# Kernel optimization log

Hardware: AMD Instinct MI355X
Metric: run time of the kernel (lower is better)

Reference implementation:

```python
import jax, jax.numpy as jnp
import numpy as np

N = 16384   # num_nodes (also in_channels: identity-style features)
C = 256     # hidden channels
K = 16      # num_classes
E = 524288  # num edges


def gcn_conv(x, src, dst, ew, W, b, num_nodes):
    """PyG GCNConv: linear transform, then sym-normalized scatter-add aggregation.
    Self-loops (weight 1) are appended; norm = d^-1/2[src] * w * d^-1/2[dst]."""
    h = x @ W                                            # [N, out]
    loop = jnp.arange(num_nodes, dtype=src.dtype)
    s = jnp.concatenate([src, loop])
    d = jnp.concatenate([dst, loop])
    w = jnp.concatenate([ew, jnp.ones((num_nodes,), ew.dtype)])
    deg = jax.ops.segment_sum(w, d, num_segments=num_nodes)
    dinv = jnp.where(deg > 0, jax.lax.rsqrt(jnp.maximum(deg, 1e-12)), 0.0)
    norm = dinv[s] * w * dinv[d]                         # [E+N]
    msg = norm[:, None] * h[s]                           # gather + scale
    out = jax.ops.segment_sum(msg, d, num_segments=num_nodes)  # scatter-add
    return out + b


def setup_inputs() -> dict:
    key = jax.random.key(0)
    k1, k2, k3, k4, k5, k6, k7 = jax.random.split(key, 7)
    x = jax.random.normal(k1, (N, N), dtype=jnp.float32)
    edge_index = jax.random.randint(k2, (2, E), 0, N, dtype=jnp.int64)
    edge_weight = jax.random.uniform(k3, (E,), dtype=jnp.float32)
    # GCNConv parameters (glorot-ish scale)
    W1 = jax.random.normal(k4, (N, C), dtype=jnp.float32) / np.sqrt(N)
    b1 = jnp.zeros((C,), jnp.float32)
    W2 = jax.random.normal(k5, (C, K), dtype=jnp.float32) / np.sqrt(C)
    b2 = jnp.zeros((K,), jnp.float32)
    return {"x": x, "edge_index": edge_index, "edge_weight": edge_weight,
            "W1": W1, "b1": b1, "W2": W2, "b2": b2}


def reference(x, edge_index, edge_weight, W1, b1, W2, b2):
    src, dst = edge_index[0], edge_index[1]
    h = gcn_conv(x, src, dst, edge_weight, W1, b1, N)
    h = jax.nn.relu(h)
    # dropout p=0.5 is identity in eval mode (self.training == False)
    out = gcn_conv(h, src, dst, edge_weight, W2, b2, N)
    return out
```

## Files before the change

kernel.cpp:

```cpp
#include <hip/hip_runtime.h>
#include <stdint.h>


namespace {
constexpr int NN = 16384;
constexpr int CH = 256;
constexpr int KC = 16;
constexpr int NE = 524288;
constexpr int KD = 16384;
constexpr int KSPLIT = 4;
constexpr int BM = 128;
constexpr int NT = KD / KSPLIT / 32;
constexpr int ABYTES = BM * 128;
constexpr int BBYTES = 256 * 64;

constexpr size_t OFF_W1T  = 0;
constexpr size_t OFF_HP   = 8388608;
constexpr size_t OFF_HB   = 75497472;
constexpr size_t OFF_OUT1 = 83886080;
constexpr size_t OFF_H2   = 100663296;
constexpr size_t OFF_DEG  = 101711872;
constexpr size_t OFF_CNT  = 101777408;
constexpr size_t OFF_DINV = 101842944;
constexpr size_t OFF_ROWP = 101908480;
constexpr size_t OFF_CUR  = 102039552;
constexpr size_t OFF_COLS = 102105088;
constexpr size_t OFF_NRM  = 104202240;
}

typedef __attribute__((ext_vector_type(8))) short bf16x8;
typedef __attribute__((ext_vector_type(4))) float f32x4;

__device__ __forceinline__ unsigned short f2bf(float f) {
  unsigned int u = __builtin_bit_cast(unsigned int, f);
  u += 0x7fffu + ((u >> 16) & 1u);
  return (unsigned short)(u >> 16);
}
__device__ __forceinline__ float bf2f(unsigned short v) {
  unsigned int u = ((unsigned int)v) << 16;
  return __builtin_bit_cast(float, u);
}

__global__ __launch_bounds__(256)
void k_w1t(const float* __restrict__ w1, unsigned short* __restrict__ w1t) {
  __shared__ float tile[64][65];
  const int t = threadIdx.x;
  const int kb = blockIdx.x * 64;
  const int nb = blockIdx.y * 64;
  const int r = t >> 6;
  const int c = t & 63;
#pragma unroll
  for (int i = 0; i < 16; ++i)
    tile[i * 4 + r][c] = w1[(size_t)(kb + i * 4 + r) * CH + nb + c];
  __syncthreads();
#pragma unroll
  for (int i = 0; i < 16; ++i)
    w1t[(size_t)(nb + i * 4 + r) * KD + kb + c] = f2bf(tile[c][i * 4 + r]);
}

__global__ __launch_bounds__(256)
void k_deg(const int* __restrict__ dst, const float* __restrict__ ew,
           float* __restrict__ deg, int* __restrict__ cnt) {
  const int e = blockIdx.x * 256 + threadIdx.x;
  const int d = dst[e];
  atomicAdd(&deg[d], ew[e]);
  atomicAdd(&cnt[d], 1);
}

__global__ __launch_bounds__(256)
void k_scan(const int* __restrict__ cnt, const float* __restrict__ deg,
            int* __restrict__ rowp, int* __restrict__ curs,
            float* __restrict__ dinv) {
  __shared__ int ps[256];
  const int t = threadIdx.x;
  const int base = t * 64;
  int s = 0;
  for (int j = 0; j < 64; ++j) s += cnt[base + j];
  ps[t] = s;
  for (int j = 0; j < 64; ++j)
    dinv[base + j] = rsqrtf(deg[base + j] + 1.0f);
  __syncthreads();
  int v = s;
  for (int off = 1; off < 256; off <<= 1) {
    int u = (t >= off) ? ps[t - off] : 0;
    __syncthreads();
    v += u;
    ps[t] = v;
    __syncthreads();
  }
  int run = v - s;
  for (int j = 0; j < 64; ++j) {
    int c = cnt[base + j];
    rowp[base + j] = run;
    curs[base + j] = run;
    run += c;
  }
  if (t == 255) rowp[NN] = run;
}

__global__ __launch_bounds__(256)
void k_fill(const int* __restrict__ src, const int* __restrict__ dst,
            const float* __restrict__ ew, const float* __restrict__ dinv,
            int* __restrict__ curs, int* __restrict__ cols, float* __restrict__ nrm) {
  const int e = blockIdx.x * 256 + threadIdx.x;
  const int s = src[e], d = dst[e];
  const int pos = atomicAdd(&curs[d], 1);
  cols[pos] = s;
  nrm[pos] = dinv[s] * ew[e] * dinv[d];
}

__global__ __launch_bounds__(512, 2)
void k_gemm1(const float* __restrict__ x, const unsigned short* __restrict__ w1t,
             float* __restrict__ hp) {
  __shared__ __align__(16) uint8_t lds[4][ABYTES + BBYTES];

  const int tid  = threadIdx.x;
  const int lane = tid & 63;
  const int wave = tid >> 6;
  const int wm   = wave >> 2;
  const int wn   = wave & 3;

  const int bid  = blockIdx.x;
  const int xcd  = bid & 7;
  const int slot = bid >> 3;
  const int kb   = xcd >> 1;
  const int bm0  = (slot * 2 + (xcd & 1)) * BM;
  const int koff = kb * (KD / KSPLIT);

  const float* asrc0 = x + (size_t)(bm0 + 8 * wave + (lane >> 3)) * KD + koff
                         + (((lane & 7) ^ (lane >> 3)) << 2);
  const float* asrc1 = asrc0 + (size_t)64 * KD;
  const unsigned short* bsrc0 = w1t + (size_t)(16 * wave + (lane >> 2)) * KD + koff
                                    + (((lane & 3) ^ ((lane >> 3) & 3)) << 3);
  const unsigned short* bsrc1 = bsrc0 + (size_t)128 * KD;

  const int fr = lane & 15, fg = lane >> 4;
  const int aoff = (((2 * fg) ^ (fr & 7)) << 4);
  const int boff = ((fg ^ ((fr >> 1) & 3)) << 4);
  const int arow = (wm * 64 + fr) * 128 + aoff;
  const int brow = ABYTES + (wn * 64 + fr) * 64 + boff;

  f32x4 acc[4][4] = {};

  auto ISSUE = [&](int tile, int buf) {
    uint8_t* base = &lds[buf][0];
    const float* ap0 = asrc0 + (size_t)tile * 32;
    const float* ap1 = asrc1 + (size_t)tile * 32;
    const unsigned short* bp0 = bsrc0 + (size_t)tile * 32;
    const unsigned short* bp1 = bsrc1 + (size_t)tile * 32;
    __builtin_amdgcn_global_load_lds(
        (const __attribute__((address_space(1))) void*)ap0,
        (__attribute__((address_space(3))) void*)(base + wave * 1024), 16, 0, 0);
    __builtin_amdgcn_global_load_lds(
        (const __attribute__((address_space(1))) void*)ap1,
        (__attribute__((address_space(3))) void*)(base + (wave + 8) * 1024), 16, 0, 0);
    __builtin_amdgcn_global_load_lds(
        (const __attribute__((address_space(1))) void*)bp0,
        (__attribute__((address_space(3))) void*)(base + ABYTES + wave * 1024), 16, 0, 0);
    __builtin_amdgcn_global_load_lds(
        (const __attribute__((address_space(1))) void*)bp1,
        (__attribute__((address_space(3))) void*)(base + ABYTES + 8192 + wave * 1024), 16, 0, 0);
  };

  ISSUE(0, 0);
  ISSUE(1, 1);
  ISSUE(2, 2);

  for (int t = 0; t < NT; ++t) {
    int t3 = t + 3; if (t3 >= NT) t3 -= NT;
    ISSUE(t3, (t + 3) & 3);
    asm volatile("s_waitcnt vmcnt(12)" ::: "memory");
    asm volatile("s_barrier" ::: "memory");
    const uint8_t* Ab = &lds[t & 3][0];
    bf16x8 bfr[4];
#pragma unroll
    for (int ni = 0; ni < 4; ++ni)
      bfr[ni] = *reinterpret_cast<const bf16x8*>(Ab + brow + ni * 1024);
    __builtin_amdgcn_s_setprio(1);
#pragma unroll
    for (int mi = 0; mi < 4; ++mi) {
      const f32x4 lo = *reinterpret_cast<const f32x4*>(Ab + arow + mi * 2048);
      const f32x4 hi = *reinterpret_cast<const f32x4*>(Ab + ((arow + mi * 2048) ^ 16));
      bf16x8 af;
      af[0] = (short)f2bf(lo[0]); af[1] = (short)f2bf(lo[1]);
      af[2] = (short)f2bf(lo[2]); af[3] = (short)f2bf(lo[3]);
      af[4] = (short)f2bf(hi[0]); af[5] = (short)f2bf(hi[1]);
      af[6] = (short)f2bf(hi[2]); af[7] = (short)f2bf(hi[3]);
#pragma unroll
      for (int ni = 0; ni < 4; ++ni)
        acc[mi][ni] = __builtin_amdgcn_mfma_f32_16x16x32_bf16(af, bfr[ni], acc[mi][ni], 0, 0, 0);
    }
    __builtin_amdgcn_s_setprio(0);
    asm volatile("s_barrier" ::: "memory");
  }

  float* hpo = hp + (size_t)kb * NN * CH;
#pragma unroll
  for (int mi = 0; mi < 4; ++mi)
#pragma unroll
    for (int ni = 0; ni < 4; ++ni)
#pragma unroll
      for (int r = 0; r < 4; ++r) {
        const int m = bm0 + wm * 64 + mi * 16 + fg * 4 + r;
        const int n = wn * 64 + ni * 16 + fr;
        hpo[(size_t)m * CH + n] = acc[mi][ni][r];
      }
}

__global__ __launch_bounds__(256)
void k_hred(const float* __restrict__ hp, unsigned short* __restrict__ hb) {
  const size_t i = ((size_t)blockIdx.x * 256 + threadIdx.x) * 8;
  float s[8];
#pragma unroll
  for (int j = 0; j < 8; ++j) s[j] = 0.f;
#pragma unroll
  for (int p = 0; p < KSPLIT; ++p) {
    const float* q = hp + (size_t)p * NN * CH + i;
    const float4 v0 = *reinterpret_cast<const float4*>(q);
    const float4 v1 = *reinterpret_cast<const float4*>(q + 4);
    s[0] += v0.x; s[1] += v0.y; s[2] += v0.z; s[3] += v0.w;
    s[4] += v1.x; s[5] += v1.y; s[6] += v1.z; s[7] += v1.w;
  }
  bf16x8 o;
#pragma unroll
  for (int j = 0; j < 8; ++j) o[j] = (short)f2bf(s[j]);
  *reinterpret_cast<bf16x8*>(hb + i) = o;
}

__global__ __launch_bounds__(256)
void k_agg1(const unsigned short* __restrict__ hb, const int* __restrict__ rowp,
            const int* __restrict__ cols, const float* __restrict__ nrm,
            const float* __restrict__ dinv, const float* __restrict__ b1,
            float* __restrict__ out1) {
  __shared__ float red[4][256];
  const int i = blockIdx.x;
  const int t = threadIdx.x;
  const int w = t >> 6, l = t & 63;
  const int beg = rowp[i], end = rowp[i + 1];
  float a0 = 0.f, a1 = 0.f, a2 = 0.f, a3 = 0.f;
  int e = beg + w;
  for (; e + 4 < end; e += 8) {
    const int s0 = cols[e], s1 = cols[e + 4];
    const float n0 = nrm[e], n1 = nrm[e + 4];
    const ushort4 h0 = *reinterpret_cast<const ushort4*>(hb + (size_t)s0 * CH + l * 4);
    const ushort4 h1 = *reinterpret_cast<const ushort4*>(hb + (size_t)s1 * CH + l * 4);
    a0 += n0 * bf2f(h0.x) + n1 * bf2f(h1.x);
    a1 += n0 * bf2f(h0.y) + n1 * bf2f(h1.y);
    a2 += n0 * bf2f(h0.z) + n1 * bf2f(h1.z);
    a3 += n0 * bf2f(h0.w) + n1 * bf2f(h1.w);
  }
  if (e < end) {
    const int s0 = cols[e];
    const float n0 = nrm[e];
    const ushort4 h0 = *reinterpret_cast<const ushort4*>(hb + (size_t)s0 * CH + l * 4);
    a0 += n0 * bf2f(h0.x); a1 += n0 * bf2f(h0.y);
    a2 += n0 * bf2f(h0.z); a3 += n0 * bf2f(h0.w);
  }
  *reinterpret_cast<float4*>(&red[w][l * 4]) = make_float4(a0, a1, a2, a3);
  __syncthreads();
  const float di = dinv[i];
  float sum = red[0][t] + red[1][t] + red[2][t] + red[3][t]
            + di * di * bf2f(hb[(size_t)i * CH + t]) + b1[t];
  out1[(size_t)i * CH + t] = fmaxf(sum, 0.0f);
}

__global__ __launch_bounds__(256)
void k_gemm2(const float* __restrict__ out1, const float* __restrict__ w2,
             float* __restrict__ h2) {
  __shared__ float xs[16][256];
  __shared__ float ws[256 * 16];
  const int t = threadIdx.x;
  const int n0 = blockIdx.x * 16;
#pragma unroll
  for (int i = 0; i < 16; ++i) ws[i * 256 + t] = w2[i * 256 + t];
#pragma unroll
  for (int i = 0; i < 16; ++i) xs[i][t] = out1[(size_t)(n0 + i) * CH + t];
  __syncthreads();
  const int node = t >> 4, k = t & 15;
  float acc = 0.f;
#pragma unroll 8
  for (int c = 0; c < 256; ++c) acc += xs[node][c] * ws[c * 16 + k];
  h2[(size_t)(n0 + node) * KC + k] = acc;
}

__global__ __launch_bounds__(256)
void k_agg2(const float* __restrict__ h2, const int* __restrict__ rowp,
            const int* __restrict__ cols, const float* __restrict__ nrm,
            const float* __restrict__ dinv, const float* __restrict__ b2,
            float* __restrict__ out) {
  const int i = blockIdx.x * 4 + (threadIdx.x >> 6);
  const int lane = threadIdx.x & 63;
  const int k = lane & 15, g = lane >> 4;
  const int beg = rowp[i], end = rowp[i + 1];
  float acc = 0.f;
  for (int e = beg + g; e < end; e += 4)
    acc += nrm[e] * h2[(size_t)cols[e] * KC + k];
  acc += __shfl_xor(acc, 16);
  acc += __shfl_xor(acc, 32);
  if (g == 0) {
    const float di = dinv[i];
    out[(size_t)i * KC + k] = acc + di * di * h2[(size_t)i * KC + k] + b2[k];
  }
}

extern "C" void kernel_launch(void* const* d_in, const int* in_sizes, int n_in,
                              void* d_out, int out_size, void* d_ws, size_t ws_size,
                              hipStream_t stream) {
  const float* x  = (const float*)d_in[0];
  const int*   ei = (const int*)d_in[1];
  const float* ew = (const float*)d_in[2];
  const float* w1 = (const float*)d_in[3];
  const float* b1 = (const float*)d_in[4];
  const float* w2 = (const float*)d_in[5];
  const float* b2 = (const float*)d_in[6];
  const int* src = ei;
  const int* dst = ei + NE;

  uint8_t* ws = (uint8_t*)d_ws;
  unsigned short* w1t = (unsigned short*)(ws + OFF_W1T);
  float* hp   = (float*)(ws + OFF_HP);
  unsigned short* hb = (unsigned short*)(ws + OFF_HB);
  float* out1 = (float*)(ws + OFF_OUT1);
  float* h2   = (float*)(ws + OFF_H2);
  float* deg  = (float*)(ws + OFF_DEG);
  int*   cnt  = (int*)(ws + OFF_CNT);
  float* dinv = (float*)(ws + OFF_DINV);
  int*   rowp = (int*)(ws + OFF_ROWP);
  int*   curs = (int*)(ws + OFF_CUR);
  int*   cols = (int*)(ws + OFF_COLS);
  float* nrm  = (float*)(ws + OFF_NRM);
  float* out  = (float*)d_out;

  hipMemsetAsync(ws + OFF_DEG, 0, 131072, stream);

  k_w1t <<<dim3(256, 4), 256, 0, stream>>>(w1, w1t);
  k_deg <<<NE / 256, 256, 0, stream>>>(dst, ew, deg, cnt);
  k_scan<<<1, 256, 0, stream>>>(cnt, deg, rowp, curs, dinv);
  k_fill<<<NE / 256, 256, 0, stream>>>(src, dst, ew, dinv, curs, cols, nrm);
  k_gemm1<<<(NN / BM) * KSPLIT, 512, 0, stream>>>(x, w1t, hp);
  k_hred<<<NN * CH / (256 * 8), 256, 0, stream>>>(hp, hb);
  k_agg1<<<NN, 256, 0, stream>>>(hb, rowp, cols, nrm, dinv, b1, out1);
  k_gemm2<<<NN / 16, 256, 0, stream>>>(out1, w2, h2);
  k_agg2<<<NN / 4, 256, 0, stream>>>(h2, rowp, cols, nrm, dinv, b2, out);
}
```

Before: 499.9 us.

## Replace LDS-staged gemm1 with direct register double-buffered fragment loads

The big x@W1 GEMM no longer stages A and B tiles through LDS with global_load_lds and barriers. Each wave now loads its MFMA fragments straight from global memory into registers, double-buffered in software, using nontemporal loads for x and nontemporal stores for the partial outputs. The block tile shrinks to 64 rows with 4 waves, launched as 1024 blocks. This removes LDS traffic and barrier sync, but each wave re-reads W1 fragments from global/L2 with no sharing across waves, and the A loads become strided rows, which may hurt coalescing on a kernel bound by streaming the 1 GB x matrix.

```diff
diff --git a/kernel.cpp b/kernel.cpp
--- a/kernel.cpp
+++ b/kernel.cpp
@@ -9,10 +9,7 @@
 constexpr int NE = 524288;
 constexpr int KD = 16384;
 constexpr int KSPLIT = 4;
-constexpr int BM = 128;
-constexpr int NT = KD / KSPLIT / 32;
-constexpr int ABYTES = BM * 128;
-constexpr int BBYTES = 256 * 64;
+constexpr int NJ = KD / KSPLIT / 32;
 
 constexpr size_t OFF_W1T  = 0;
 constexpr size_t OFF_HP   = 8388608;
@@ -109,101 +106,82 @@
   nrm[pos] = dinv[s] * ew[e] * dinv[d];
 }
 
-__global__ __launch_bounds__(512, 2)
+struct Frag {
+  f32x4 a[4];
+  bf16x8 b[8];
+};
+
+__global__ __launch_bounds__(256, 2)
 void k_gemm1(const float* __restrict__ x, const unsigned short* __restrict__ w1t,
              float* __restrict__ hp) {
-  __shared__ __align__(16) uint8_t lds[4][ABYTES + BBYTES];
-
   const int tid  = threadIdx.x;
   const int lane = tid & 63;
   const int wave = tid >> 6;
-  const int wm   = wave >> 2;
-  const int wn   = wave & 3;
+  const int wm   = wave >> 1;
+  const int wn   = wave & 1;
 
   const int bid  = blockIdx.x;
   const int xcd  = bid & 7;
   const int slot = bid >> 3;
   const int kb   = xcd >> 1;
-  const int bm0  = (slot * 2 + (xcd & 1)) * BM;
+  const int bm0  = (slot * 2 + (xcd & 1)) * 64;
   const int koff = kb * (KD / KSPLIT);
 
-  const float* asrc0 = x + (size_t)(bm0 + 8 * wave + (lane >> 3)) * KD + koff
-                         + (((lane & 7) ^ (lane >> 3)) << 2);
-  const float* asrc1 = asrc0 + (size_t)64 * KD;
-  const unsigned short* bsrc0 = w1t + (size_t)(16 * wave + (lane >> 2)) * KD + koff
-                                    + (((lane & 3) ^ ((lane >> 3) & 3)) << 3);
-  const unsigned short* bsrc1 = bsrc0 + (size_t)128 * KD;
-
   const int fr = lane & 15, fg = lane >> 4;
-  const int aoff = (((2 * fg) ^ (fr & 7)) << 4);
-  const int boff = ((fg ^ ((fr >> 1) & 3)) << 4);
-  const int arow = (wm * 64 + fr) * 128 + aoff;
-  const int brow = ABYTES + (wn * 64 + fr) * 64 + boff;
-
-  f32x4 acc[4][4] = {};
-
-  auto ISSUE = [&](int tile, int buf) {
-    uint8_t* base = &lds[buf][0];
-    const float* ap0 = asrc0 + (size_t)tile * 32;
-    const float* ap1 = asrc1 + (size_t)tile * 32;
-    const unsigned short* bp0 = bsrc0 + (size_t)tile * 32;
-    const unsigned short* bp1 = bsrc1 + (size_t)tile * 32;
-    __builtin_amdgcn_global_load_lds(
-        (const __attribute__((address_space(1))) void*)ap0,
-        (__attribute__((address_space(3))) void*)(base + wave * 1024), 16, 0, 0);
-    __builtin_amdgcn_global_load_lds(
-        (const __attribute__((address_space(1))) void*)ap1,
-        (__attribute__((address_space(3))) void*)(base + (wave + 8) * 1024), 16, 0, 0);
-    __builtin_amdgcn_global_load_lds(
-        (const __attribute__((address_space(1))) void*)bp0,
-        (__attribute__((address_space(3))) void*)(base + ABYTES + wave * 1024), 16, 0, 0);
-    __builtin_amdgcn_global_load_lds(
-        (const __attribute__((address_space(1))) void*)bp1,
-        (__attribute__((address_space(3))) void*)(base + ABYTES + 8192 + wave * 1024), 16, 0, 0);
+
+  const float* aP = x + (size_t)(bm0 + wm * 32 + fr) * KD + koff + fg * 8;
+  const unsigned short* bP = w1t + (size_t)(wn * 128 + fr) * KD + koff + fg * 8;
+
+  f32x4 acc[2][8] = {};
+
+  auto LOAD = [&](int j, Frag& f) {
+    const float* ap = aP + j * 32;
+#pragma unroll
+    for (int mi = 0; mi < 2; ++mi) {
+      const float* r = ap + (size_t)(mi * 16) * KD;
+      f.a[mi * 2 + 0] = __builtin_nontemporal_load(reinterpret_cast<const f32x4*>(r));
+      f.a[mi * 2 + 1] = __builtin_nontemporal_load(reinterpret_cast<const f32x4*>(r + 4));
+    }
+    const unsigned short* bp = bP + j * 32;
+#pragma unroll
+    for (int ni = 0; ni < 8; ++ni)
+      f.b[ni] = *reinterpret_cast<const bf16x8*>(bp + (size_t)(ni * 16) * KD);
   };
-
-  ISSUE(0, 0);
-  ISSUE(1, 1);
-  ISSUE(2, 2);
-
-  for (int t = 0; t < NT; ++t) {
-    int t3 = t + 3; if (t3 >= NT) t3 -= NT;
-    ISSUE(t3, (t + 3) & 3);
-    asm volatile("s_waitcnt vmcnt(12)" ::: "memory");
-    asm volatile("s_barrier" ::: "memory");
-    const uint8_t* Ab = &lds[t & 3][0];
-    bf16x8 bfr[4];
-#pragma unroll
-    for (int ni = 0; ni < 4; ++ni)
-      bfr[ni] = *reinterpret_cast<const bf16x8*>(Ab + brow + ni * 1024);
-    __builtin_amdgcn_s_setprio(1);
-#pragma unroll
-    for (int mi = 0; mi < 4; ++mi) {
-      const f32x4 lo = *reinterpret_cast<const f32x4*>(Ab + arow + mi * 2048);
-      const f32x4 hi = *reinterpret_cast<const f32x4*>(Ab + ((arow + mi * 2048) ^ 16));
-      bf16x8 af;
-      af[0] = (short)f2bf(lo[0]); af[1] = (short)f2bf(lo[1]);
-      af[2] = (short)f2bf(lo[2]); af[3] = (short)f2bf(lo[3]);
-      af[4] = (short)f2bf(hi[0]); af[5] = (short)f2bf(hi[1]);
-      af[6] = (short)f2bf(hi[2]); af[7] = (short)f2bf(hi[3]);
-#pragma unroll
-      for (int ni = 0; ni < 4; ++ni)
-        acc[mi][ni] = __builtin_amdgcn_mfma_f32_16x16x32_bf16(af, bfr[ni], acc[mi][ni], 0, 0, 0);
+  auto COMPUTE = [&](const Frag& f) {
+#pragma unroll
+    for (int mi = 0; mi < 2; ++mi) {
+      const f32x4 lo = f.a[mi * 2 + 0];
+      const f32x4 hi = f.a[mi * 2 + 1];
+      bf16x8 am;
+      am[0] = (short)f2bf(lo[0]); am[1] = (short)f2bf(lo[1]);
+      am[2] = (short)f2bf(lo[2]); am[3] = (short)f2bf(lo[3]);
+      am[4] = (short)f2bf(hi[0]); am[5] = (short)f2bf(hi[1]);
+      am[6] = (short)f2bf(hi[2]); am[7] = (short)f2bf(hi[3]);
+#pragma unroll
+      for (int ni = 0; ni < 8; ++ni)
+        acc[mi][ni] = __builtin_amdgcn_mfma_f32_16x16x32_bf16(am, f.b[ni], acc[mi][ni], 0, 0, 0);
     }
-    __builtin_amdgcn_s_setprio(0);
-    asm volatile("s_barrier" ::: "memory");
+  };
+
+  Frag s0, s1;
+  LOAD(0, s0);
+  for (int j = 0; j < NJ; j += 2) {
+    if (j + 1 < NJ) LOAD(j + 1, s1);
+    COMPUTE(s0);
+    if (j + 2 < NJ) LOAD(j + 2, s0);
+    if (j + 1 < NJ) COMPUTE(s1);
   }
 
   float* hpo = hp + (size_t)kb * NN * CH;
 #pragma unroll
-  for (int mi = 0; mi < 4; ++mi)
-#pragma unroll
-    for (int ni = 0; ni < 4; ++ni)
+  for (int mi = 0; mi < 2; ++mi)
+#pragma unroll
+    for (int ni = 0; ni < 8; ++ni)
 #pragma unroll
       for (int r = 0; r < 4; ++r) {
-        const int m = bm0 + wm * 64 + mi * 16 + fg * 4 + r;
-        const int n = wn * 64 + ni * 16 + fr;
-        hpo[(size_t)m * CH + n] = acc[mi][ni][r];
+        const int m = bm0 + wm * 32 + mi * 16 + fg * 4 + r;
+        const int n = wn * 128 + ni * 16 + fr;
+        __builtin_nontemporal_store(acc[mi][ni][r], &hpo[(size_t)m * CH + n]);
       }
 }
 
@@ -337,7 +315,7 @@
   k_deg <<<NE / 256, 256, 0, stream>>>(dst, ew, deg, cnt);
   k_scan<<<1, 256, 0, stream>>>(cnt, deg, rowp, curs, dinv);
   k_fill<<<NE / 256, 256, 0, stream>>>(src, dst, ew, dinv, curs, cols, nrm);
-  k_gemm1<<<(NN / BM) * KSPLIT, 512, 0, stream>>>(x, w1t, hp);
+  k_gemm1<<<1024, 256, 0, stream>>>(x, w1t, hp);
   k_hred<<<NN * CH / (256 * 8), 256, 0, stream>>>(hp, hb);
   k_agg1<<<NN, 256, 0, stream>>>(hb, rowp, cols, nrm, dinv, b1, out1);
   k_gemm2<<<NN / 16, 256, 0, stream>>>(out1, w2, h2);
```

Result: slower. 1.024 ms (+104.9%).
